# Performance work log

Hardware: AMD Instinct MI355X
Metric: run time of the kernel (lower is better)

Reference implementation:

```python
import jax, jax.numpy as jnp
import numpy as np

HIDDEN = 2880
NUM_HEADS = 64
NUM_KV_HEADS = 8
HEAD_DIM = 64
ROPE_THETA = 150000.0
WINDOW = 128  # sliding window size (attend to last WINDOW tokens incl. current)
SCALE = HEAD_DIM ** -0.5
Q_SIZE = NUM_HEADS * HEAD_DIM          # 4096
KV_SIZE = NUM_KV_HEADS * HEAD_DIM      # 512


def _rope_neox(x, positions):
    # x: [T, n_heads, HEAD_DIM]; neox-style rotary over the full head dim
    half = HEAD_DIM // 2
    inv_freq = 1.0 / (ROPE_THETA ** (jnp.arange(half, dtype=jnp.float32) / half))
    freqs = positions.astype(jnp.float32)[:, None] * inv_freq[None, :]  # [T, half]
    cos = jnp.cos(freqs)[:, None, :]
    sin = jnp.sin(freqs)[:, None, :]
    x1, x2 = x[..., :half], x[..., half:]
    return jnp.concatenate([x1 * cos - x2 * sin, x2 * cos + x1 * sin], axis=-1)


def setup_inputs() -> dict:
    key = jax.random.key(0)
    k1, k2, k3, k4 = jax.random.split(key, 4)
    T = 2048
    hidden_states = jax.random.normal(k1, (T, HIDDEN), dtype=jnp.float32)
    positions = jnp.arange(T, dtype=jnp.int32)
    w_qkv = jax.random.normal(k2, (HIDDEN, Q_SIZE + 2 * KV_SIZE), dtype=jnp.float32) * (HIDDEN ** -0.5)
    w_o = jax.random.normal(k3, (Q_SIZE, HIDDEN), dtype=jnp.float32) * (Q_SIZE ** -0.5)
    sinks = jax.random.normal(k4, (NUM_HEADS,), dtype=jnp.float32)
    return {"positions": positions, "hidden_states": hidden_states,
            "w_qkv": w_qkv, "w_o": w_o, "sinks": sinks}


def reference(positions, hidden_states, w_qkv, w_o, sinks):
    T = hidden_states.shape[0]
    qkv = hidden_states @ w_qkv  # [T, 5120]
    q = qkv[:, :Q_SIZE].reshape(T, NUM_HEADS, HEAD_DIM)
    k = qkv[:, Q_SIZE:Q_SIZE + KV_SIZE].reshape(T, NUM_KV_HEADS, HEAD_DIM)
    v = qkv[:, Q_SIZE + KV_SIZE:].reshape(T, NUM_KV_HEADS, HEAD_DIM)

    q = _rope_neox(q, positions)
    k = _rope_neox(k, positions)

    # GQA: each group of NUM_HEADS//NUM_KV_HEADS query heads shares one kv head
    rep = NUM_HEADS // NUM_KV_HEADS
    k = jnp.repeat(k, rep, axis=1)  # [T, NUM_HEADS, HEAD_DIM]
    v = jnp.repeat(v, rep, axis=1)

    scores = jnp.einsum('qhd,khd->hqk', q, k) * SCALE  # [H, T, T]
    pos_q = positions[:, None]
    pos_k = positions[None, :]
    mask = (pos_k <= pos_q) & (pos_q - pos_k < WINDOW)  # causal + sliding window
    neg = jnp.finfo(scores.dtype).min
    scores = jnp.where(mask[None, :, :], scores, neg)

    # softmax with per-head learned sink logit included in the denominator
    m = jnp.maximum(scores.max(axis=-1), sinks[:, None])      # [H, T]
    e = jnp.exp(scores - m[..., None])                        # [H, T, T]
    denom = e.sum(axis=-1) + jnp.exp(sinks[:, None] - m)      # [H, T]
    probs = e / denom[..., None]

    attn = jnp.einsum('hqk,khd->qhd', probs, v).reshape(T, Q_SIZE)
    return attn @ w_o  # [T, HIDDEN]
```

## Files before the change

### kernel.cpp

```cpp
#include <hip/hip_runtime.h>
#include <hip/hip_bf16.h>

#define T_SEQ   2048
#define HIDDEN  2880
#define NQ      64
#define NKV     8
#define HD      64
#define QSIZE   4096
#define KVSIZE  512
#define QKV_N   5120
#define WINDOW  128
#define SCALE_F 0.125f
#define ROPE_L2 0.53733241958f

typedef unsigned short u16;
typedef __attribute__((ext_vector_type(8))) short short8;
typedef __attribute__((ext_vector_type(4))) float f32x4;

__device__ __forceinline__ u16 f2bf(float f) {
  __hip_bfloat16 b = __float2bfloat16(f);
  u16 u; __builtin_memcpy(&u, &b, 2); return u;
}

__device__ __forceinline__ void gload16(const u16* g, u16* l) {
  __builtin_amdgcn_global_load_lds(
      (const __attribute__((address_space(1))) void*)g,
      (__attribute__((address_space(3))) void*)l, 16, 0, 0);
}

#define CAST_BLKS 5760
#define TQ_BX 80
#define TQ_BLKS (80 * 45)
#define PREP_BLKS (CAST_BLKS + TQ_BLKS)

__global__ void prep_kernel(const float* __restrict__ hidden,
                            const float* __restrict__ w_qkv,
                            u16* __restrict__ Xb, u16* __restrict__ Wqt) {
  __shared__ float tile[64][65];
  const int b = blockIdx.x, tid = threadIdx.x;
  if (b < CAST_BLKS) {
    size_t i = (size_t)b * 256 + tid;
    float4 v = ((const float4*)hidden)[i];
    ushort4 o;
    o.x = f2bf(v.x); o.y = f2bf(v.y); o.z = f2bf(v.z); o.w = f2bf(v.w);
    ((ushort4*)Xb)[i] = o;
    return;
  }
  const int bb = b - CAST_BLKS;
  const int bx = bb % TQ_BX, by = bb / TQ_BX;
  const int r0 = by * 64, c0 = bx * 64;
  const int tx = tid & 15, ty = tid >> 4;
#pragma unroll
  for (int i = 0; i < 4; ++i) {
    float4 v = *(const float4*)(w_qkv + (size_t)(r0 + ty + 16 * i) * QKV_N + c0 + tx * 4);
    tile[tx * 4 + 0][ty + 16 * i] = v.x;
    tile[tx * 4 + 1][ty + 16 * i] = v.y;
    tile[tx * 4 + 2][ty + 16 * i] = v.z;
    tile[tx * 4 + 3][ty + 16 * i] = v.w;
  }
  __syncthreads();
  const int rr8 = (tid & 7) * 8, cc0 = tid >> 3;
#pragma unroll
  for (int p = 0; p < 2; ++p) {
    int cc = cc0 + 32 * p;
    short8 o;
#pragma unroll
    for (int j = 0; j < 8; ++j) o[j] = (short)f2bf(tile[cc][rr8 + j]);
    *(short8*)(Wqt + (size_t)(c0 + cc) * HIDDEN + r0 + rr8) = o;
  }
}

template <int MODE>
__global__ __launch_bounds__(256)
void gemm_bt_kernel(const u16* __restrict__ A, const u16* __restrict__ B,
                    float* __restrict__ Cout, const int* __restrict__ positions,
                    u16* __restrict__ qb, u16* __restrict__ kb,
                    u16* __restrict__ vb, const float* __restrict__ tin,
                    u16* __restrict__ tout, int Kstride, int NKT,
                    int Bvalid, int Nout, int ldc, int NX, int NYC, int NY,
                    int GEMM_BLKS) {
  __shared__ __align__(16) u16 smem[2 * (64 + 128) * 64];
  const int tid = threadIdx.x;
  const int bb = blockIdx.x;

  if (MODE == 1 && bb >= GEMM_BLKS) {
    float (*tile)[65] = (float (*)[65])smem;
    const int bt = bb - GEMM_BLKS;
    const int bx = bt % 45, by = bt / 45;
    const int r0 = by * 64, c0 = bx * 64;
    const int tx = tid & 15, ty = tid >> 4;
#pragma unroll
    for (int i = 0; i < 4; ++i) {
      float4 v = *(const float4*)(tin + (size_t)(r0 + ty + 16 * i) * HIDDEN + c0 + tx * 4);
      tile[tx * 4 + 0][ty + 16 * i] = v.x;
      tile[tx * 4 + 1][ty + 16 * i] = v.y;
      tile[tx * 4 + 2][ty + 16 * i] = v.z;
      tile[tx * 4 + 3][ty + 16 * i] = v.w;
    }
    __syncthreads();
    const int rr8 = (tid & 7) * 8, cc0 = tid >> 3;
#pragma unroll
    for (int p = 0; p < 2; ++p) {
      int cc = cc0 + 32 * p;
      short8 o;
#pragma unroll
      for (int j = 0; j < 8; ++j) o[j] = (short)f2bf(tile[cc][rr8 + j]);
      *(short8*)(tout + (size_t)(c0 + cc) * QSIZE + r0 + rr8) = o;
    }
    return;
  }

  const int xcd = bb & 7, bi = bb >> 3;
  const int ny = xcd * NYC + (bi % NYC);
  const int mx = bi / NYC;
  if (ny >= NY || mx >= NX) return;
  const int m0 = mx * 64, n0 = ny * 128;

  const int lane = tid & 63, wave = tid >> 6;
  const int quad = lane >> 4, l16 = lane & 15;
  const int wm = wave >> 1, wn = wave & 1;

  const int NB = (64 + 128) * 64;
  u16* As = smem;
  u16* Bs = smem + 64 * 64;

  const u16* Aptr[2]; const u16* Bptr[4]; u16* Alds[2]; u16* Blds[4];
#pragma unroll
  for (int it = 0; it < 2; ++it) {
    int c = it * 256 + tid;
    int r = c >> 3;
    int lcol = ((c & 7) ^ (r & 7)) * 8;
    Aptr[it] = A + (size_t)(m0 + r) * Kstride + lcol;
    Alds[it] = As + c * 8;
  }
#pragma unroll
  for (int it = 0; it < 4; ++it) {
    int c = it * 256 + tid;
    int r = c >> 3;
    int lcol = ((c & 7) ^ (r & 7)) * 8;
    int br = n0 + r; br = br < Bvalid ? br : Bvalid - 1;
    Bptr[it] = B + (size_t)br * Kstride + lcol;
    Blds[it] = Bs + c * 8;
  }

  f32x4 acc[2][4] = {};
  const int sw0 = (quad ^ (l16 & 7)) * 8;

#pragma unroll
  for (int it = 0; it < 2; ++it) gload16(Aptr[it], Alds[it]);
#pragma unroll
  for (int it = 0; it < 4; ++it) gload16(Bptr[it], Blds[it]);
  asm volatile("s_waitcnt vmcnt(0)" ::: "memory");
  __syncthreads();

  int cur = 0;
  for (int t = 0; t < NKT; ++t) {
    if (t + 1 < NKT) {
      const int bo = (cur ^ 1) * NB;
      const int ktn = (t + 1) * 64;
#pragma unroll
      for (int it = 0; it < 2; ++it) gload16(Aptr[it] + ktn, Alds[it] + bo);
#pragma unroll
      for (int it = 0; it < 4; ++it) gload16(Bptr[it] + ktn, Blds[it] + bo);
    }
    const u16* Ac = As + cur * NB;
    const u16* Bc = Bs + cur * NB;
#pragma unroll
    for (int kk = 0; kk < 2; ++kk) {
      const int swo = sw0 ^ (kk * 32);
      short8 af[2], bf[4];
#pragma unroll
      for (int i = 0; i < 2; ++i)
        af[i] = *(const short8*)(Ac + (wm * 32 + i * 16 + l16) * 64 + swo);
#pragma unroll
      for (int j = 0; j < 4; ++j)
        bf[j] = *(const short8*)(Bc + (wn * 64 + j * 16 + l16) * 64 + swo);
#pragma unroll
      for (int i = 0; i < 2; ++i)
#pragma unroll
        for (int j = 0; j < 4; ++j)
          acc[i][j] = __builtin_amdgcn_mfma_f32_16x16x32_bf16(af[i], bf[j], acc[i][j], 0, 0, 0);
    }
    if (t + 1 < NKT) {
      asm volatile("s_waitcnt vmcnt(0)" ::: "memory");
      __syncthreads();
      cur ^= 1;
    }
  }

  if (MODE == 0) {
#pragma unroll
    for (int i = 0; i < 2; ++i) {
      const int row = m0 + wm * 32 + i * 16 + quad * 4;
#pragma unroll
      for (int j = 0; j < 4; ++j) {
        const int col = n0 + wn * 64 + j * 16 + l16;
        if (col < Nout)
#pragma unroll
          for (int r = 0; r < 4; ++r)
            Cout[(size_t)(row + r) * ldc + col] = acc[i][j][r];
      }
    }
  } else {
    const int region = (n0 < QSIZE) ? 0 : (n0 < QSIZE + KVSIZE ? 1 : 2);
    if (region <= 1) {
      float invs[2];
#pragma unroll
      for (int j = 0; j < 2; ++j)
        invs[j] = exp2f(-(float)(j * 16 + l16) * ROPE_L2);
#pragma unroll
      for (int i = 0; i < 2; ++i) {
#pragma unroll
        for (int r = 0; r < 4; ++r) {
          const int row = m0 + wm * 32 + i * 16 + quad * 4 + r;
          const float pos = (float)positions[row];
#pragma unroll
          for (int j = 0; j < 2; ++j) {
            float s, c;
            sincosf(pos * invs[j], &s, &c);
            const float x1 = acc[i][j][r], x2 = acc[i][j + 2][r];
            const float o1 = x1 * c - x2 * s, o2 = x2 * c + x1 * s;
            const int col = n0 + wn * 64 + j * 16 + l16;
            if (region == 0) {
              qb[(size_t)row * QSIZE + col] = f2bf(o1);
              qb[(size_t)row * QSIZE + col + 32] = f2bf(o2);
            } else {
              kb[(size_t)row * KVSIZE + col - QSIZE] = f2bf(o1);
              kb[(size_t)row * KVSIZE + col - QSIZE + 32] = f2bf(o2);
            }
          }
        }
      }
    } else {
#pragma unroll
      for (int i = 0; i < 2; ++i) {
        const int row = m0 + wm * 32 + i * 16 + quad * 4;
#pragma unroll
        for (int j = 0; j < 4; ++j) {
          const int col = n0 + wn * 64 + j * 16 + l16 - (QSIZE + KVSIZE);
#pragma unroll
          for (int r = 0; r < 4; ++r)
            vb[(size_t)(row + r) * KVSIZE + col] = f2bf(acc[i][j][r]);
        }
      }
    }
  }
}

__global__ __launch_bounds__(256, 2)
void attn_kernel(const u16* __restrict__ qb, const u16* __restrict__ kb,
                 const u16* __restrict__ vb, const float* __restrict__ sinks,
                 u16* __restrict__ attnb) {
  __shared__ __align__(16) u16 Ks[160 * 72];
  __shared__ __align__(16) u16 Vt[64 * 164];
  __shared__ __align__(16) u16 Pb[4 * 16 * 164];
  const int qt = blockIdx.x, g = blockIdx.y;
  const int q0 = qt * 32, kstart = q0 - 128;
  const int tid = threadIdx.x;
  const int lane = tid & 63, wave = tid >> 6;
  const int quad = lane >> 4, l16 = lane & 15;

  for (int s = tid; s < 1280; s += 256) {
    int r = s >> 3, c8 = (s & 7) * 8;
    int tg = kstart + r; tg = tg < 0 ? 0 : tg;
    *(short8*)(Ks + r * 72 + c8) =
        *(const short8*)(kb + (size_t)tg * KVSIZE + g * HD + c8);
  }
  {
    const u16* vbase = vb + g * HD;
#pragma unroll
    for (int it = 0; it < 5; ++it) {
      int s = it * 256 + tid;
      int r = s >> 3, c8 = (s & 7) * 8;
      int tg = kstart + r; tg = tg < 0 ? 0 : tg;
      gload16(vbase + (size_t)tg * KVSIZE + c8, Pb + s * 8);
    }
  }
  asm volatile("s_waitcnt vmcnt(0)" ::: "memory");
  __syncthreads();

  short8 bk[10][2];
#pragma unroll
  for (int jf = 0; jf < 10; ++jf)
#pragma unroll
    for (int kk = 0; kk < 2; ++kk)
      bk[jf][kk] = *(const short8*)(Ks + (jf * 16 + l16) * 72 + kk * 32 + quad * 8);

  for (int s = tid; s < 1280; s += 256) {
    int k8 = s >> 6, d = s & 63;
    short8 tmp;
#pragma unroll
    for (int j = 0; j < 8; ++j) tmp[j] = (short)Pb[(k8 * 8 + j) * 64 + d];
    *(short8*)(Vt + d * 164 + k8 * 8) = tmp;
  }
  __syncthreads();

  const int strip = wave & 1, hb = wave >> 1;
  const int qrow0 = q0 + strip * 16;
  u16* Pw = Pb + wave * 16 * 164;
  for (int hh = 0; hh < 4; ++hh) {
    const int h = g * 8 + hb + hh * 2;
    short8 aq[2];
#pragma unroll
    for (int kk = 0; kk < 2; ++kk)
      aq[kk] = *(const short8*)(qb + (size_t)(qrow0 + l16) * QSIZE + h * HD + kk * 32 + quad * 8);
    f32x4 sc[10];
#pragma unroll
    for (int jf = 0; jf < 10; ++jf) {
      f32x4 c = {0.f, 0.f, 0.f, 0.f};
#pragma unroll
      for (int kk = 0; kk < 2; ++kk)
        c = __builtin_amdgcn_mfma_f32_16x16x32_bf16(aq[kk], bk[jf][kk], c, 0, 0, 0);
      sc[jf] = c;
    }

    const float sink = sinks[h];
    float pinv[4];
#pragma unroll
    for (int r = 0; r < 4; ++r) {
      const int qg = qrow0 + quad * 4 + r;
      float mx = -3.0e38f;
#pragma unroll
      for (int jf = 0; jf < 10; ++jf) {
        int kg = kstart + jf * 16 + l16;
        bool valid = (kg >= 0) && (kg <= qg) && (qg - kg < WINDOW);
        float sv = valid ? sc[jf][r] * SCALE_F : -3.0e38f;
        sc[jf][r] = sv;
        mx = fmaxf(mx, sv);
      }
#pragma unroll
      for (int d = 1; d < 16; d <<= 1) mx = fmaxf(mx, __shfl_xor(mx, d, 64));
      mx = fmaxf(mx, sink);
      float sum = 0.f;
#pragma unroll
      for (int jf = 0; jf < 10; ++jf) {
        float e = __expf(sc[jf][r] - mx);
        sc[jf][r] = e;
        sum += e;
      }
#pragma unroll
      for (int d = 1; d < 16; d <<= 1) sum += __shfl_xor(sum, d, 64);
      sum += __expf(sink - mx);
      pinv[r] = 1.0f / sum;
    }

#pragma unroll
    for (int jf = 0; jf < 10; ++jf)
#pragma unroll
      for (int r = 0; r < 4; ++r)
        Pw[(quad * 4 + r) * 164 + jf * 16 + l16] = f2bf(sc[jf][r] * pinv[r]);

    f32x4 o[4] = {};
#pragma unroll
    for (int kk = 0; kk < 5; ++kk) {
      short8 ap = *(const short8*)(Pw + l16 * 164 + kk * 32 + quad * 8);
#pragma unroll
      for (int jf = 0; jf < 4; ++jf) {
        short8 bv = *(const short8*)(Vt + (jf * 16 + l16) * 164 + kk * 32 + quad * 8);
        o[jf] = __builtin_amdgcn_mfma_f32_16x16x32_bf16(ap, bv, o[jf], 0, 0, 0);
      }
    }
#pragma unroll
    for (int jf = 0; jf < 4; ++jf)
#pragma unroll
      for (int r = 0; r < 4; ++r) {
        int qg = qrow0 + quad * 4 + r;
        attnb[(size_t)qg * QSIZE + h * HD + jf * 16 + l16] = f2bf(o[jf][r]);
      }
  }
}

extern "C" void kernel_launch(void* const* d_in, const int* in_sizes, int n_in,
                              void* d_out, int out_size, void* d_ws, size_t ws_size,
                              hipStream_t stream) {
  (void)in_sizes; (void)n_in; (void)out_size; (void)ws_size;
  const int*   positions = (const int*)d_in[0];
  const float* hidden    = (const float*)d_in[1];
  const float* w_qkv     = (const float*)d_in[2];
  const float* w_o       = (const float*)d_in[3];
  const float* sinks     = (const float*)d_in[4];

  char* p = (char*)d_ws;
  u16* Xb    = (u16*)p; p += (size_t)T_SEQ * HIDDEN * 2;
  u16* Wqt   = (u16*)p; p += (size_t)QKV_N * HIDDEN * 2;
  u16* Wot   = (u16*)p; p += (size_t)HIDDEN * QSIZE * 2;
  u16* qb    = (u16*)p; p += (size_t)T_SEQ * QSIZE * 2;
  u16* kb    = (u16*)p; p += (size_t)T_SEQ * KVSIZE * 2;
  u16* vb    = (u16*)p; p += (size_t)T_SEQ * KVSIZE * 2;
  u16* attnb = (u16*)p; p += (size_t)T_SEQ * QSIZE * 2;

  prep_kernel<<<PREP_BLKS, 256, 0, stream>>>(hidden, w_qkv, Xb, Wqt);
  gemm_bt_kernel<1><<<32 * 8 * 5 + 45 * 64, 256, 0, stream>>>(
      Xb, Wqt, nullptr, positions, qb, kb, vb, w_o, Wot,
      HIDDEN, 45, QKV_N, QKV_N, QKV_N, 32, 5, 40, 32 * 8 * 5);
  attn_kernel<<<dim3(T_SEQ / 32, NKV), 256, 0, stream>>>(qb, kb, vb, sinks, attnb);
  gemm_bt_kernel<0><<<32 * 8 * 3, 256, 0, stream>>>(
      attnb, Wot, (float*)d_out, nullptr, nullptr, nullptr, nullptr,
      nullptr, nullptr, QSIZE, 64, HIDDEN, HIDDEN, HIDDEN, 32, 3, 23, 32 * 8 * 3);
}
```

Baseline: 313.1 us.

## Store V transposed from QKV GEMM epilogue and load directly into attention LDS

The QKV GEMM epilogue now writes V in a [dim, token] layout using packed 4-element stores. The attention kernel can then copy V straight into its transposed LDS buffer, which removes the staging pass through Pb, the per-element LDS transpose loop, the explicit vmcnt wait and one barrier. The change also raises wave priority with s_setprio around the two MFMA sections. The cost is less coalesced 8-byte scattered stores in the GEMM epilogue for the V tile.

```diff
diff --git a/kernel.cpp b/kernel.cpp
--- a/kernel.cpp
+++ b/kernel.cpp
@@ -238,9 +238,12 @@
 #pragma unroll
         for (int j = 0; j < 4; ++j) {
           const int col = n0 + wn * 64 + j * 16 + l16 - (QSIZE + KVSIZE);
-#pragma unroll
-          for (int r = 0; r < 4; ++r)
-            vb[(size_t)(row + r) * KVSIZE + col] = f2bf(acc[i][j][r]);
+          ushort4 pk;
+          pk.x = f2bf(acc[i][j][0]);
+          pk.y = f2bf(acc[i][j][1]);
+          pk.z = f2bf(acc[i][j][2]);
+          pk.w = f2bf(acc[i][j][3]);
+          *(ushort4*)(vb + (size_t)col * T_SEQ + row) = pk;
         }
       }
     }
@@ -249,7 +252,7 @@
 
 __global__ __launch_bounds__(256, 2)
 void attn_kernel(const u16* __restrict__ qb, const u16* __restrict__ kb,
-                 const u16* __restrict__ vb, const float* __restrict__ sinks,
+                 const u16* __restrict__ vb_t, const float* __restrict__ sinks,
                  u16* __restrict__ attnb) {
   __shared__ __align__(16) u16 Ks[160 * 72];
   __shared__ __align__(16) u16 Vt[64 * 164];
@@ -267,16 +270,15 @@
         *(const short8*)(kb + (size_t)tg * KVSIZE + g * HD + c8);
   }
   {
-    const u16* vbase = vb + g * HD;
+    const int d = tid >> 2, q4 = tid & 3;
+    const u16* vrow = vb_t + (size_t)(g * HD + d) * T_SEQ;
 #pragma unroll
     for (int it = 0; it < 5; ++it) {
-      int s = it * 256 + tid;
-      int r = s >> 3, c8 = (s & 7) * 8;
-      int tg = kstart + r; tg = tg < 0 ? 0 : tg;
-      gload16(vbase + (size_t)tg * KVSIZE + c8, Pb + s * 8);
-    }
-  }
-  asm volatile("s_waitcnt vmcnt(0)" ::: "memory");
+      int k0 = (q4 * 5 + it) * 8;
+      int cs = kstart + k0; cs = cs < 0 ? 0 : cs;
+      *(short8*)(Vt + d * 164 + k0) = *(const short8*)(vrow + cs);
+    }
+  }
   __syncthreads();
 
   short8 bk[10][2];
@@ -285,15 +287,6 @@
 #pragma unroll
     for (int kk = 0; kk < 2; ++kk)
       bk[jf][kk] = *(const short8*)(Ks + (jf * 16 + l16) * 72 + kk * 32 + quad * 8);
-
-  for (int s = tid; s < 1280; s += 256) {
-    int k8 = s >> 6, d = s & 63;
-    short8 tmp;
-#pragma unroll
-    for (int j = 0; j < 8; ++j) tmp[j] = (short)Pb[(k8 * 8 + j) * 64 + d];
-    *(short8*)(Vt + d * 164 + k8 * 8) = tmp;
-  }
-  __syncthreads();
 
   const int strip = wave & 1, hb = wave >> 1;
   const int qrow0 = q0 + strip * 16;
@@ -305,6 +298,7 @@
     for (int kk = 0; kk < 2; ++kk)
       aq[kk] = *(const short8*)(qb + (size_t)(qrow0 + l16) * QSIZE + h * HD + kk * 32 + quad * 8);
     f32x4 sc[10];
+    __builtin_amdgcn_s_setprio(1);
 #pragma unroll
     for (int jf = 0; jf < 10; ++jf) {
       f32x4 c = {0.f, 0.f, 0.f, 0.f};
@@ -313,6 +307,7 @@
         c = __builtin_amdgcn_mfma_f32_16x16x32_bf16(aq[kk], bk[jf][kk], c, 0, 0, 0);
       sc[jf] = c;
     }
+    __builtin_amdgcn_s_setprio(0);
 
     const float sink = sinks[h];
     float pinv[4];
@@ -351,6 +346,7 @@
         Pw[(quad * 4 + r) * 164 + jf * 16 + l16] = f2bf(sc[jf][r] * pinv[r]);
 
     f32x4 o[4] = {};
+    __builtin_amdgcn_s_setprio(1);
 #pragma unroll
     for (int kk = 0; kk < 5; ++kk) {
       short8 ap = *(const short8*)(Pw + l16 * 164 + kk * 32 + quad * 8);
@@ -360,6 +356,7 @@
         o[jf] = __builtin_amdgcn_mfma_f32_16x16x32_bf16(ap, bv, o[jf], 0, 0, 0);
       }
     }
+    __builtin_amdgcn_s_setprio(0);
 #pragma unroll
     for (int jf = 0; jf < 4; ++jf)
 #pragma unroll
@@ -386,14 +383,14 @@
   u16* Wot   = (u16*)p; p += (size_t)HIDDEN * QSIZE * 2;
   u16* qb    = (u16*)p; p += (size_t)T_SEQ * QSIZE * 2;
   u16* kb    = (u16*)p; p += (size_t)T_SEQ * KVSIZE * 2;
-  u16* vb    = (u16*)p; p += (size_t)T_SEQ * KVSIZE * 2;
+  u16* vbt   = (u16*)p; p += (size_t)T_SEQ * KVSIZE * 2;
   u16* attnb = (u16*)p; p += (size_t)T_SEQ * QSIZE * 2;
 
   prep_kernel<<<PREP_BLKS, 256, 0, stream>>>(hidden, w_qkv, Xb, Wqt);
   gemm_bt_kernel<1><<<32 * 8 * 5 + 45 * 64, 256, 0, stream>>>(
-      Xb, Wqt, nullptr, positions, qb, kb, vb, w_o, Wot,
+      Xb, Wqt, nullptr, positions, qb, kb, vbt, w_o, Wot,
       HIDDEN, 45, QKV_N, QKV_N, QKV_N, 32, 5, 40, 32 * 8 * 5);
-  attn_kernel<<<dim3(T_SEQ / 32, NKV), 256, 0, stream>>>(qb, kb, vb, sinks, attnb);
+  attn_kernel<<<dim3(T_SEQ / 32, NKV), 256, 0, stream>>>(qb, kb, vbt, sinks, attnb);
   gemm_bt_kernel<0><<<32 * 8 * 3, 256, 0, stream>>>(
       attnb, Wot, (float*)d_out, nullptr, nullptr, nullptr, nullptr,
       nullptr, nullptr, QSIZE, 64, HIDDEN, HIDDEN, HIDDEN, 32, 3, 23, 32 * 8 * 3);
```

New measurement: 315.4 us, median of 5. No clear change (+0.7%).
